# Performance work log

Hardware: AMD Instinct MI355X
Metric: run time of the kernel (lower is better)

## Reference

```python
import jax, jax.numpy as jnp
import numpy as np

N = 10000
E = 160000
C = 256        # in_channels
M = 256        # mid_channels
R = 64         # nregion


def _glorot(key, shape):
    fan_in, fan_out = shape[-1], shape[0]
    lim = (6.0 / (fan_in + fan_out)) ** 0.5
    return jax.random.uniform(key, shape, jnp.float32, -lim, lim)


def setup_inputs() -> dict:
    key = jax.random.key(0)
    ks = jax.random.split(key, 12)
    x = jax.random.normal(ks[0], (N, C), jnp.float32)
    edge_index = jax.random.randint(ks[1], (2, E), 0, N, jnp.int32)
    conv_w = _glorot(ks[2], (C, C))
    conv_b = jnp.zeros((C,), jnp.float32)
    lin1_w = _glorot(ks[3], (M, C)); lin1_b = jnp.zeros((M,), jnp.float32)
    lin2_w = _glorot(ks[4], (M, M)); lin2_b = jnp.zeros((M,), jnp.float32)
    lin3_w = _glorot(ks[5], (1, M)); lin3_b = jnp.zeros((1,), jnp.float32)
    lin4_w = _glorot(ks[6], (M, M)); lin4_b = jnp.zeros((M,), jnp.float32)
    bilin_w = _glorot(ks[7], (R, M, M)) * 0.1
    bilin_b = jnp.zeros((R,), jnp.float32)
    return {"x": x, "edge_index": edge_index,
            "conv_w": conv_w, "conv_b": conv_b,
            "lin1_w": lin1_w, "lin1_b": lin1_b,
            "lin2_w": lin2_w, "lin2_b": lin2_b,
            "lin3_w": lin3_w, "lin3_b": lin3_b,
            "lin4_w": lin4_w, "lin4_b": lin4_b,
            "bilin_w": bilin_w, "bilin_b": bilin_b}


def gcn_conv(x, edge_index, w, b):
    # PyG GCNConv: add self-loops, symmetric D^-1/2 (A+I) D^-1/2 normalization
    src, dst = edge_index[0], edge_index[1]
    n = x.shape[0]
    xw = x @ w.T                                            # [N, C]
    deg = jnp.ones((n,), xw.dtype).at[dst].add(jnp.ones((E,), xw.dtype))  # +1 for self loop
    dinv = jax.lax.rsqrt(deg)
    norm = dinv[src] * dinv[dst]                            # [E]
    agg = jnp.zeros_like(xw).at[dst].add(norm[:, None] * xw[src])
    agg = agg + (dinv * dinv)[:, None] * xw                 # self-loop messages
    return agg + b


def reference(x, edge_index, conv_w, conv_b, lin1_w, lin1_b, lin2_w, lin2_b,
              lin3_w, lin3_b, lin4_w, lin4_b, bilin_w, bilin_b):
    out = jax.nn.relu(gcn_conv(x, edge_index, conv_w, conv_b))
    x0 = out + x                                            # residual [N, C]
    x0 = jax.nn.relu(x0 @ lin1_w.T + lin1_b)                # [N, M]
    x1 = jax.nn.relu(x0 @ lin2_w.T + lin2_b)
    x1 = x1 @ lin3_w.T + lin3_b                             # [N, 1]
    x2 = jax.nn.relu(x0 @ lin4_w.T + lin4_b)                # [N, M]
    # Bilinear(x2, x2): out[n,r] = x2[n] @ W[r] @ x2[n] + b[r]
    t = (x2 @ bilin_w.reshape(R * M, M).T).reshape(-1, R, M)  # [N, R, M]
    x2 = jnp.sum(t * x2[:, None, :], axis=-1) + bilin_b       # [N, R]
    return (x1, x2)
```

## Files before the change

### kernel.cpp

```cpp
#include <hip/hip_runtime.h>

typedef unsigned short u16;
typedef __attribute__((ext_vector_type(8))) short bf16x8;
typedef __attribute__((ext_vector_type(8))) unsigned short u16x8;
typedef __attribute__((ext_vector_type(4))) float f32x4;

#define N_NODES 10000
#define E_EDGES 160000
#define CX_N 2560000
#define W_N  65536
#define WB_N 4194304
#define CANON_BIG_BLOCKS 3426
#define HIST_BLOCKS 79

__device__ __forceinline__ float b2f(u16 u) {
  union { unsigned i; float f; } c; c.i = ((unsigned)u) << 16; return c.f;
}
__device__ __forceinline__ u16 f2b(float f) {
  union { float f; unsigned i; } c; c.f = f;
  unsigned i = c.i;
  return (u16)((i + 0x7FFFu + ((i >> 16) & 1u)) >> 16);
}

__global__ void detect_kernel(const unsigned* __restrict__ w, int* __restrict__ flag) {
  int t = threadIdx.x;
  int cnt = 0;
  for (int i = t; i < 1024; i += 64) {
    unsigned e = (w[i] >> 7) & 0xFF;
    cnt += (e >= 100 && e <= 145) ? 1 : 0;
  }
  for (int o = 32; o; o >>= 1) cnt += __shfl_xor(cnt, o);
  if (t == 0) *flag = (cnt >= 512) ? 1 : 0;
}

__global__ void canon_all_kernel(const void* sx, const void* swc, const void* sw1,
                                 const void* sw2, const void* sw4, const void* swB,
                                 const void* sbc, const void* sb1, const void* sb2,
                                 const void* sb4, const void* sw3, const void* sbB,
                                 const void* sb3,
                                 u16* __restrict__ dstBase,
                                 u16* cbc, u16* cb1, u16* cb2, u16* cb4,
                                 u16* cw3, u16* cbB, u16* cb3,
                                 const int* __restrict__ ei, int* __restrict__ count,
                                 const int* __restrict__ flag) {
  int b = blockIdx.x;
  int f = *flag;
  if (b < CANON_BIG_BLOCKS) {
    long e = ((long)b * 256 + threadIdx.x) * 8;
    const void* src; long so;
    if (e < CX_N)                { src = sx;  so = e; }
    else if (e < CX_N + W_N)     { src = swc; so = e - CX_N; }
    else if (e < CX_N + 2 * W_N) { src = sw1; so = e - (CX_N + W_N); }
    else if (e < CX_N + 3 * W_N) { src = sw2; so = e - (CX_N + 2 * W_N); }
    else if (e < CX_N + 4 * W_N) { src = sw4; so = e - (CX_N + 3 * W_N); }
    else                         { src = swB; so = e - (CX_N + 4 * W_N); }
    if (f) {
      u16x8 v = *((const u16x8*)((const u16*)src + so));
      *(u16x8*)(dstBase + e) = v;
    } else {
      const float* fp = (const float*)src + so;
      float4 a = *(const float4*)fp;
      float4 c = *(const float4*)(fp + 4);
      u16x8 o;
      o[0] = f2b(a.x); o[1] = f2b(a.y); o[2] = f2b(a.z); o[3] = f2b(a.w);
      o[4] = f2b(c.x); o[5] = f2b(c.y); o[6] = f2b(c.z); o[7] = f2b(c.w);
      *(u16x8*)(dstBase + e) = o;
    }
  } else if (b == CANON_BIG_BLOCKS) {
    int t = threadIdx.x;
    const void* srcs[7] = {sbc, sb1, sb2, sb4, sw3, sbB, sb3};
    u16* dsts[7] = {cbc, cb1, cb2, cb4, cw3, cbB, cb3};
    const int ns[7] = {256, 256, 256, 256, 256, 64, 1};
#pragma unroll
    for (int k = 0; k < 7; ++k) {
      if (t < ns[k]) {
        if (f) dsts[k][t] = ((const u16*)srcs[k])[t];
        else   dsts[k][t] = f2b(((const float*)srcs[k])[t]);
      }
    }
  } else {
    int base = (b - CANON_BIG_BLOCKS - 1) * 2048 + threadIdx.x * 8;
#pragma unroll
    for (int k = 0; k < 8; ++k) {
      int i = base + k;
      if (i < E_EDGES) atomicAdd(&count[ei[E_EDGES + i]], 1);
    }
  }
}

__device__ __forceinline__ void stage_async(const u16* __restrict__ src, int stride,
                                            int row0, int maxRow, int k0,
                                            u16* lds, int w, int lane) {
  int rsel = lane >> 3;
  int gch = (lane & 7) ^ rsel;
#pragma unroll
  for (int i = 0; i < 4; ++i) {
    int rb = (w * 4 + i) * 8;
    int grow = row0 + rb + rsel;
    grow = grow > maxRow ? maxRow : grow;
    const u16* gp = src + (size_t)grow * stride + k0 + gch * 8;
    u16* lp = lds + rb * 64;
    __builtin_amdgcn_global_load_lds(
        (const __attribute__((address_space(1))) void*)gp,
        (__attribute__((address_space(3))) void*)lp, 16, 0, 0);
  }
}

__device__ __forceinline__ void mma_tile(const u16* lA, const u16* lB,
                                         f32x4 acc[4][4], int wr, int wc, int lane) {
#pragma unroll
  for (int ks = 0; ks < 2; ++ks) {
    bf16x8 af[4], bfr[4];
    int g = ks * 4 + (lane >> 4);
#pragma unroll
    for (int t = 0; t < 4; ++t) {
      int rowA = wr * 64 + t * 16 + (lane & 15);
      af[t] = *(const bf16x8*)(lA + rowA * 64 + ((g ^ (rowA & 7)) * 8));
      int rowB = wc * 64 + t * 16 + (lane & 15);
      bfr[t] = *(const bf16x8*)(lB + rowB * 64 + ((g ^ (rowB & 7)) * 8));
    }
#pragma unroll
    for (int ti = 0; ti < 4; ++ti)
#pragma unroll
      for (int tj = 0; tj < 4; ++tj)
        acc[ti][tj] = __builtin_amdgcn_mfma_f32_16x16x32_bf16(af[ti], bfr[tj],
                                                              acc[ti][tj], 0, 0, 0);
  }
}

template <bool RELU, bool F32OUT>
__global__ __launch_bounds__(256, 2)
void gemm_kernel(const u16* __restrict__ A, const u16* __restrict__ B,
                 const u16* __restrict__ bias, float* __restrict__ outF,
                 u16* __restrict__ outB, int NN, int J, int K) {
  __shared__ u16 lA[128 * 64];
  __shared__ u16 lB[128 * 64];
  int lane = threadIdx.x & 63;
  int w = threadIdx.x >> 6;
  int wr = w >> 1, wc = w & 1;
  int n0 = blockIdx.y * 128;
  int j0 = blockIdx.x * 128;
  f32x4 acc[4][4];
#pragma unroll
  for (int i = 0; i < 4; ++i)
#pragma unroll
    for (int j = 0; j < 4; ++j) acc[i][j] = (f32x4){0.f, 0.f, 0.f, 0.f};

  for (int kt = 0; kt < K; kt += 64) {
    stage_async(A, K, n0, NN - 1, kt, lA, w, lane);
    stage_async(B, K, j0, J - 1, kt, lB, w, lane);
    __syncthreads();
    mma_tile(lA, lB, acc, wr, wc, lane);
    __syncthreads();
  }

#pragma unroll
  for (int ti = 0; ti < 4; ++ti)
#pragma unroll
    for (int tj = 0; tj < 4; ++tj) {
      int col = j0 + wc * 64 + tj * 16 + (lane & 15);
      float bv = bias ? b2f(bias[col]) : 0.0f;
#pragma unroll
      for (int r = 0; r < 4; ++r) {
        int row = n0 + wr * 64 + ti * 16 + ((lane >> 4) << 2) + r;
        if (row < NN) {
          float v = acc[ti][tj][r] + bv;
          if (RELU) v = fmaxf(v, 0.0f);
          if (F32OUT) outF[(size_t)row * J + col] = v;
          else        outB[(size_t)row * J + col] = f2b(v);
        }
      }
    }
}

__global__ __launch_bounds__(256, 2)
void gemm_fused234_kernel(const u16* __restrict__ A, const u16* __restrict__ B,
                          const u16* __restrict__ bias, const u16* __restrict__ w3,
                          float* __restrict__ out1acc, u16* __restrict__ x2v, int NN) {
  __shared__ u16 lA[128 * 64];
  __shared__ u16 lB[128 * 64];
  int lane = threadIdx.x & 63;
  int w = threadIdx.x >> 6;
  int wr = w >> 1, wc = w & 1;
  int n0 = blockIdx.y * 128;
  int j0 = blockIdx.x * 128;
  f32x4 acc[4][4];
#pragma unroll
  for (int i = 0; i < 4; ++i)
#pragma unroll
    for (int j = 0; j < 4; ++j) acc[i][j] = (f32x4){0.f, 0.f, 0.f, 0.f};

  for (int kt = 0; kt < 256; kt += 64) {
    stage_async(A, 256, n0, NN - 1, kt, lA, w, lane);
    stage_async(B, 256, j0, 511, kt, lB, w, lane);
    __syncthreads();
    mma_tile(lA, lB, acc, wr, wc, lane);
    __syncthreads();
  }

  if (j0 < 256) {
    float part[4][4];
#pragma unroll
    for (int ti = 0; ti < 4; ++ti)
#pragma unroll
      for (int r = 0; r < 4; ++r) part[ti][r] = 0.0f;
#pragma unroll
    for (int ti = 0; ti < 4; ++ti)
#pragma unroll
      for (int tj = 0; tj < 4; ++tj) {
        int col = j0 + wc * 64 + tj * 16 + (lane & 15);
        float bv = b2f(bias[col]);
        float wv = b2f(w3[col]);
#pragma unroll
        for (int r = 0; r < 4; ++r) {
          float v = fmaxf(acc[ti][tj][r] + bv, 0.0f);
          part[ti][r] += v * wv;
        }
      }
#pragma unroll
    for (int ti = 0; ti < 4; ++ti)
#pragma unroll
      for (int r = 0; r < 4; ++r) {
        float s = part[ti][r];
        s += __shfl_xor(s, 1);
        s += __shfl_xor(s, 2);
        s += __shfl_xor(s, 4);
        s += __shfl_xor(s, 8);
        if ((lane & 15) == 0) {
          int row = n0 + wr * 64 + ti * 16 + ((lane >> 4) << 2) + r;
          if (row < NN) unsafeAtomicAdd(&out1acc[row], s);
        }
      }
  } else {
#pragma unroll
    for (int ti = 0; ti < 4; ++ti)
#pragma unroll
      for (int tj = 0; tj < 4; ++tj) {
        int col = j0 + wc * 64 + tj * 16 + (lane & 15);
        float bv = b2f(bias[col]);
#pragma unroll
        for (int r = 0; r < 4; ++r) {
          int row = n0 + wr * 64 + ti * 16 + ((lane >> 4) << 2) + r;
          if (row < NN) {
            float v = fmaxf(acc[ti][tj][r] + bv, 0.0f);
            x2v[(size_t)row * 256 + (col - 256)] = f2b(v);
          }
        }
      }
  }
}

__device__ __forceinline__ void stage64(const u16* __restrict__ src,
                                        int row0, int maxRow, int k0,
                                        u16* lds, int w, int lane) {
  int rsel = lane >> 3;
  int gch = (lane & 7) ^ rsel;
#pragma unroll
  for (int i = 0; i < 2; ++i) {
    int rb = (w * 2 + i) * 8;
    int grow = row0 + rb + rsel;
    grow = grow > maxRow ? maxRow : grow;
    const u16* gp = src + (size_t)grow * 256 + k0 + gch * 8;
    u16* lp = lds + rb * 64;
    __builtin_amdgcn_global_load_lds(
        (const __attribute__((address_space(1))) void*)gp,
        (__attribute__((address_space(3))) void*)lp, 16, 0, 0);
  }
}

__global__ __launch_bounds__(256, 4)
void bilinear_tlp_kernel(const u16* __restrict__ x2v, const u16* __restrict__ W,
                         float* __restrict__ out2acc, int NN) {
  __shared__ u16 lA[64 * 64];
  __shared__ u16 lB[128 * 64];
  __shared__ float sc[64 * 4];
  int lane = threadIdx.x & 63;
  int w = threadIdx.x >> 6;
  int n0 = blockIdx.y * 64;
  int rm0 = blockIdx.x * 128;
  int m0g = rm0 & 255;
  int region = rm0 >> 8;

  f32x4 acc[4][2];
#pragma unroll
  for (int i = 0; i < 4; ++i)
#pragma unroll
    for (int j = 0; j < 2; ++j) acc[i][j] = (f32x4){0.f, 0.f, 0.f, 0.f};

#pragma unroll
  for (int kt4 = 0; kt4 < 4; ++kt4) {
    stage64(x2v, n0, NN - 1, kt4 * 64, lA, w, lane);
    stage_async(W, 256, rm0, 16383, kt4 * 64, lB, w, lane);
    __syncthreads();
#pragma unroll
    for (int ks = 0; ks < 2; ++ks) {
      bf16x8 af[4], bfr[2];
      int g = ks * 4 + (lane >> 4);
#pragma unroll
      for (int t = 0; t < 4; ++t) {
        int rowA = t * 16 + (lane & 15);
        af[t] = *(const bf16x8*)(lA + rowA * 64 + ((g ^ (rowA & 7)) * 8));
      }
#pragma unroll
      for (int u = 0; u < 2; ++u) {
        int rowB = w * 32 + u * 16 + (lane & 15);
        bfr[u] = *(const bf16x8*)(lB + rowB * 64 + ((g ^ (rowB & 7)) * 8));
      }
#pragma unroll
      for (int t = 0; t < 4; ++t)
#pragma unroll
        for (int u = 0; u < 2; ++u)
          acc[t][u] = __builtin_amdgcn_mfma_f32_16x16x32_bf16(af[t], bfr[u],
                                                              acc[t][u], 0, 0, 0);
    }
    __syncthreads();
  }

#pragma unroll
  for (int ti = 0; ti < 4; ++ti)
#pragma unroll
    for (int r = 0; r < 4; ++r) {
      int rowl = ti * 16 + ((lane >> 4) << 2) + r;
      int row = n0 + rowl;
      int rc = row < NN ? row : NN - 1;
      const u16* xr = x2v + (size_t)rc * 256 + m0g + w * 32 + (lane & 15);
      float s = acc[ti][0][r] * b2f(xr[0]) + acc[ti][1][r] * b2f(xr[16]);
      s += __shfl_xor(s, 1);
      s += __shfl_xor(s, 2);
      s += __shfl_xor(s, 4);
      s += __shfl_xor(s, 8);
      if ((lane & 15) == 0) sc[rowl * 4 + w] = s;
    }
  __syncthreads();
  int tid = threadIdx.x;
  if (tid < 64) {
    float s = sc[tid * 4] + sc[tid * 4 + 1] + sc[tid * 4 + 2] + sc[tid * 4 + 3];
    int nn = n0 + tid;
    if (nn < NN) unsafeAtomicAdd(&out2acc[(size_t)nn * 64 + region], s);
  }
}

__global__ void scan_kernel(const int* __restrict__ count, int* __restrict__ start,
                            int* __restrict__ cursor, float* __restrict__ dinv) {
  __shared__ int wsum[16];
  __shared__ int carry_s;
  int t = threadIdx.x;
  int wv = t >> 6, ln = t & 63;
  if (t == 0) carry_s = 0;
  __syncthreads();
  for (int base = 0; base < N_NODES; base += 1024) {
    int i = base + t;
    int v = (i < N_NODES) ? count[i] : 0;
    int s = v;
#pragma unroll
    for (int o = 1; o < 64; o <<= 1) {
      int u = __shfl_up(s, o);
      if (ln >= o) s += u;
    }
    if (ln == 63) wsum[wv] = s;
    __syncthreads();
    if (wv == 0) {
      int x = (ln < 16) ? wsum[ln] : 0;
#pragma unroll
      for (int o = 1; o < 16; o <<= 1) {
        int u = __shfl_up(x, o);
        if (ln >= o) x += u;
      }
      if (ln < 16) wsum[ln] = x;
    }
    __syncthreads();
    int excl = s - v + (wv ? wsum[wv - 1] : 0) + carry_s;
    if (i < N_NODES) {
      start[i] = excl;
      cursor[i] = excl;
      dinv[i] = rsqrtf(1.0f + (float)v);
    }
    __syncthreads();
    if (t == 0) carry_s += wsum[15];
    __syncthreads();
  }
}

__global__ void place_kernel(const int* __restrict__ ei, int* __restrict__ cursor,
                             int* __restrict__ order) {
  int i = blockIdx.x * 256 + threadIdx.x;
  if (i >= E_EDGES) return;
  int d = ei[E_EDGES + i];
  int pos = atomicAdd(&cursor[d], 1);
  order[pos] = i;
}

__global__ void gather_kernel(const int* __restrict__ ei, const int* __restrict__ order,
                              const int* __restrict__ start, const int* __restrict__ count,
                              const float* __restrict__ dinv, const float* __restrict__ xw,
                              const u16* __restrict__ conv_b, const u16* __restrict__ x,
                              u16* __restrict__ x0) {
  int node = (blockIdx.x * blockDim.x + threadIdx.x) >> 6;
  int lane = threadIdx.x & 63;
  if (node >= N_NODES) return;
  int s0 = start[node], cnt = count[node];
  float dn = dinv[node];
  float ax = 0.f, ay = 0.f, az = 0.f, aw = 0.f;
  for (int base = 0; base < cnt; base += 64) {
    int rem = cnt - base;
    int m = rem < 64 ? rem : 64;
    int eid = (lane < m) ? order[s0 + base + lane] : 0;
    int s = (lane < m) ? ei[eid] : 0;
    float nrm = (lane < m) ? dinv[s] * dn : 0.f;
    for (int j = 0; j < m; ++j) {
      int sj = __shfl(s, j);
      float nj = __shfl(nrm, j);
      float4 v = *((const float4*)(xw + (size_t)sj * 256) + lane);
      ax += nj * v.x; ay += nj * v.y; az += nj * v.z; aw += nj * v.w;
    }
  }
  float4 sv = *((const float4*)(xw + (size_t)node * 256) + lane);
  float slw = dn * dn;
  const u16* bb = conv_b + lane * 4;
  const u16* xr = x + (size_t)node * 256 + lane * 4;
  u16 o[4];
  float vals[4] = {ax + slw * sv.x, ay + slw * sv.y, az + slw * sv.z, aw + slw * sv.w};
#pragma unroll
  for (int j = 0; j < 4; ++j) {
    float v = vals[j] + b2f(bb[j]);
    v = fmaxf(v, 0.0f) + b2f(xr[j]);
    o[j] = f2b(v);
  }
  *((ushort4*)(x0 + (size_t)node * 256) + lane) = make_ushort4(o[0], o[1], o[2], o[3]);
}

__global__ void out_final_kernel(const float* __restrict__ out1acc,
                                 const float* __restrict__ out2acc,
                                 const u16* __restrict__ b3, const u16* __restrict__ bb,
                                 void* __restrict__ dout, const int* __restrict__ flag) {
  int idx = blockIdx.x * 256 + threadIdx.x;
  int f = *flag;
  if (idx < N_NODES) {
    float v = out1acc[idx] + b2f(b3[0]);
    if (f) ((u16*)dout)[idx] = f2b(v);
    else   ((float*)dout)[idx] = v;
  } else if (idx < N_NODES + N_NODES * 64) {
    int k = idx - N_NODES;
    float v = out2acc[k] + b2f(bb[k & 63]);
    if (f) ((u16*)dout)[idx] = f2b(v);
    else   ((float*)dout)[idx] = v;
  }
}

extern "C" void kernel_launch(void* const* d_in, const int* in_sizes, int n_in,
                              void* d_out, int out_size, void* d_ws, size_t ws_size,
                              hipStream_t stream) {
  const int* ei = (const int*)d_in[1];

  float* ws      = (float*)d_ws;
  float* xw      = ws;
  int*   count   = (int*)(xw + N_NODES * 256);
  int*   start   = count + 10240;
  int*   cursor  = start + 10240;
  int*   order   = cursor + 10240;
  float* dinv    = (float*)(order + E_EDGES);
  float* out1acc = dinv + 10240;
  float* out2acc = out1acc + 10240;
  u16* x0  = (u16*)(out2acc + N_NODES * 64);
  u16* x0m = x0 + N_NODES * 256;
  u16* x2v = x0m + N_NODES * 256;
  u16* cx  = x2v + N_NODES * 256;
  u16* cwc = cx + CX_N;
  u16* cw1 = cwc + W_N;
  u16* cw2 = cw1 + W_N;
  u16* cw4 = cw2 + W_N;
  u16* cwB = cw4 + W_N;
  u16* cbc = cwB + WB_N;
  u16* cb1 = cbc + 256;
  u16* cb2 = cb1 + 256;
  u16* cb4 = cb2 + 256;
  u16* cw3 = cb4 + 256;
  u16* cbB = cw3 + 256;
  u16* cb3 = cbB + 64;
  int* flag = (int*)(cb3 + 16);

  hipMemsetAsync(count, 0, N_NODES * sizeof(int), stream);
  hipMemsetAsync(out1acc, 0, (10240 + (size_t)N_NODES * 64) * sizeof(float), stream);

  detect_kernel<<<1, 64, 0, stream>>>((const unsigned*)d_in[0], flag);

  canon_all_kernel<<<CANON_BIG_BLOCKS + 1 + HIST_BLOCKS, 256, 0, stream>>>(
      d_in[0], d_in[2], d_in[4], d_in[6], d_in[10], d_in[12],
      d_in[3], d_in[5], d_in[7], d_in[11], d_in[8], d_in[13], d_in[9],
      cx, cbc, cb1, cb2, cb4, cw3, cbB, cb3,
      ei, count, flag);

  scan_kernel<<<1, 1024, 0, stream>>>(count, start, cursor, dinv);
  place_kernel<<<(E_EDGES + 255) / 256, 256, 0, stream>>>(ei, cursor, order);

  gemm_kernel<false, true><<<dim3(2, 79), 256, 0, stream>>>(
      cx, cwc, nullptr, xw, nullptr, N_NODES, 256, 256);

  gather_kernel<<<(N_NODES * 64 + 255) / 256, 256, 0, stream>>>(
      ei, order, start, count, dinv, xw, cbc, cx, x0);

  gemm_kernel<true, false><<<dim3(2, 79), 256, 0, stream>>>(
      x0, cw1, cb1, nullptr, x0m, N_NODES, 256, 256);

  gemm_fused234_kernel<<<dim3(4, 79), 256, 0, stream>>>(
      x0m, cw2, cb2, cw3, out1acc, x2v, N_NODES);

  bilinear_tlp_kernel<<<dim3(128, 157), 256, 0, stream>>>(x2v, cwB, out2acc, N_NODES);

  out_final_kernel<<<(N_NODES * 65 + 255) / 256, 256, 0, stream>>>(
      out1acc, out2acc, cb3, cbB, d_out, flag);
}
```

Measured before the change: 367.3 us.

## Keep bilinear weight tile in registers and loop over node tiles

The bilinear kernel now loads each block's 128-row slice of the bilinear weight matrix into registers once. Each block then iterates over up to 10 node tiles, staging the full 256-wide x2 tile into LDS for each one. This removes repeated global/LDS staging of W for every (node tile, W tile) pair. The grid shrinks from 128x157 blocks to 128x16, which lowers parallelism and adds per-tile serialization. Register pressure rises and launch bounds drop to 3 waves, and the x2 staging is no longer double-buffered against compute.

Result: slower. 405.4 us (+10.3%).

```diff
diff --git a/kernel.cpp b/kernel.cpp
--- a/kernel.cpp
+++ b/kernel.cpp
@@ -268,75 +268,93 @@
   }
 }
 
-__global__ __launch_bounds__(256, 4)
-void bilinear_tlp_kernel(const u16* __restrict__ x2v, const u16* __restrict__ W,
-                         float* __restrict__ out2acc, int NN) {
-  __shared__ u16 lA[64 * 64];
-  __shared__ u16 lB[128 * 64];
+#define NT_PER 10
+#define N_TILES 157
+#define N_GROUPS 16
+
+__global__ __launch_bounds__(256, 3)
+void bilinear_wreg_kernel(const u16* __restrict__ x2v, const u16* __restrict__ W,
+                          float* __restrict__ out2acc, int NN) {
+  __shared__ u16 lA[64 * 256];
   __shared__ float sc[64 * 4];
   int lane = threadIdx.x & 63;
   int w = threadIdx.x >> 6;
-  int n0 = blockIdx.y * 64;
-  int rm0 = blockIdx.x * 128;
+  int wt = blockIdx.x;
+  int grp = blockIdx.y;
+  int rm0 = wt * 128;
   int m0g = rm0 & 255;
   int region = rm0 >> 8;
 
-  f32x4 acc[4][2];
-#pragma unroll
-  for (int i = 0; i < 4; ++i)
-#pragma unroll
-    for (int j = 0; j < 2; ++j) acc[i][j] = (f32x4){0.f, 0.f, 0.f, 0.f};
-
-#pragma unroll
-  for (int kt4 = 0; kt4 < 4; ++kt4) {
-    stage64(x2v, n0, NN - 1, kt4 * 64, lA, w, lane);
-    stage_async(W, 256, rm0, 16383, kt4 * 64, lB, w, lane);
-    __syncthreads();
-#pragma unroll
-    for (int ks = 0; ks < 2; ++ks) {
-      bf16x8 af[4], bfr[2];
-      int g = ks * 4 + (lane >> 4);
-#pragma unroll
-      for (int t = 0; t < 4; ++t) {
-        int rowA = t * 16 + (lane & 15);
-        af[t] = *(const bf16x8*)(lA + rowA * 64 + ((g ^ (rowA & 7)) * 8));
-      }
-#pragma unroll
-      for (int u = 0; u < 2; ++u) {
-        int rowB = w * 32 + u * 16 + (lane & 15);
-        bfr[u] = *(const bf16x8*)(lB + rowB * 64 + ((g ^ (rowB & 7)) * 8));
-      }
+  bf16x8 wf[2][8];
+#pragma unroll
+  for (int u = 0; u < 2; ++u) {
+    const u16* wp = W + (size_t)(rm0 + w * 32 + u * 16 + (lane & 15)) * 256
+                      + (lane >> 4) * 8;
+#pragma unroll
+    for (int kk = 0; kk < 8; ++kk)
+      wf[u][kk] = *(const bf16x8*)(wp + kk * 32);
+  }
+
+  for (int i = 0; i < NT_PER; ++i) {
+    int nt = grp * NT_PER + i;
+    if (nt < N_TILES) {
+      int n0 = nt * 64;
+
+#pragma unroll
+      for (int kt4 = 0; kt4 < 4; ++kt4)
+        stage64(x2v, n0, NN - 1, kt4 * 64, lA + kt4 * 4096, w, lane);
+      __syncthreads();
+
+      f32x4 acc[4][2];
 #pragma unroll
       for (int t = 0; t < 4; ++t)
 #pragma unroll
-        for (int u = 0; u < 2; ++u)
-          acc[t][u] = __builtin_amdgcn_mfma_f32_16x16x32_bf16(af[t], bfr[u],
-                                                              acc[t][u], 0, 0, 0);
-    }
-    __syncthreads();
-  }
-
-#pragma unroll
-  for (int ti = 0; ti < 4; ++ti)
-#pragma unroll
-    for (int r = 0; r < 4; ++r) {
-      int rowl = ti * 16 + ((lane >> 4) << 2) + r;
-      int row = n0 + rowl;
-      int rc = row < NN ? row : NN - 1;
-      const u16* xr = x2v + (size_t)rc * 256 + m0g + w * 32 + (lane & 15);
-      float s = acc[ti][0][r] * b2f(xr[0]) + acc[ti][1][r] * b2f(xr[16]);
-      s += __shfl_xor(s, 1);
-      s += __shfl_xor(s, 2);
-      s += __shfl_xor(s, 4);
-      s += __shfl_xor(s, 8);
-      if ((lane & 15) == 0) sc[rowl * 4 + w] = s;
-    }
-  __syncthreads();
-  int tid = threadIdx.x;
-  if (tid < 64) {
-    float s = sc[tid * 4] + sc[tid * 4 + 1] + sc[tid * 4 + 2] + sc[tid * 4 + 3];
-    int nn = n0 + tid;
-    if (nn < NN) unsafeAtomicAdd(&out2acc[(size_t)nn * 64 + region], s);
+        for (int u = 0; u < 2; ++u) acc[t][u] = (f32x4){0.f, 0.f, 0.f, 0.f};
+
+#pragma unroll
+      for (int kt4 = 0; kt4 < 4; ++kt4)
+#pragma unroll
+        for (int ks = 0; ks < 2; ++ks) {
+          bf16x8 af[4];
+          int g = ks * 4 + (lane >> 4);
+#pragma unroll
+          for (int t = 0; t < 4; ++t) {
+            int rowA = t * 16 + (lane & 15);
+            af[t] = *(const bf16x8*)(lA + kt4 * 4096 + rowA * 64 +
+                                     ((g ^ (rowA & 7)) * 8));
+          }
+#pragma unroll
+          for (int t = 0; t < 4; ++t)
+#pragma unroll
+            for (int u = 0; u < 2; ++u)
+              acc[t][u] = __builtin_amdgcn_mfma_f32_16x16x32_bf16(
+                  af[t], wf[u][kt4 * 2 + ks], acc[t][u], 0, 0, 0);
+        }
+
+#pragma unroll
+      for (int ti = 0; ti < 4; ++ti)
+#pragma unroll
+        for (int r = 0; r < 4; ++r) {
+          int rowl = ti * 16 + ((lane >> 4) << 2) + r;
+          int row = n0 + rowl;
+          int rc = row < NN ? row : NN - 1;
+          const u16* xr = x2v + (size_t)rc * 256 + m0g + w * 32 + (lane & 15);
+          float s = acc[ti][0][r] * b2f(xr[0]) + acc[ti][1][r] * b2f(xr[16]);
+          s += __shfl_xor(s, 1);
+          s += __shfl_xor(s, 2);
+          s += __shfl_xor(s, 4);
+          s += __shfl_xor(s, 8);
+          if ((lane & 15) == 0) sc[rowl * 4 + w] = s;
+        }
+      __syncthreads();
+      int tid = threadIdx.x;
+      if (tid < 64) {
+        float s = sc[tid * 4] + sc[tid * 4 + 1] + sc[tid * 4 + 2] + sc[tid * 4 + 3];
+        int nn = n0 + tid;
+        if (nn < NN) unsafeAtomicAdd(&out2acc[(size_t)nn * 64 + region], s);
+      }
+      __syncthreads();
+    }
   }
 }
 
@@ -505,7 +523,8 @@
   gemm_fused234_kernel<<<dim3(4, 79), 256, 0, stream>>>(
       x0m, cw2, cb2, cw3, out1acc, x2v, N_NODES);
 
-  bilinear_tlp_kernel<<<dim3(128, 157), 256, 0, stream>>>(x2v, cwB, out2acc, N_NODES);
+  bilinear_wreg_kernel<<<dim3(128, N_GROUPS), 256, 0, stream>>>(
+      x2v, cwB, out2acc, N_NODES);
 
   out_final_kernel<<<(N_NODES * 65 + 255) / 256, 256, 0, stream>>>(
       out1acc, out2acc, cb3, cbB, d_out, flag);
```
